# Optimization experiments

Measured on AMD Instinct MI355X. Metric: run time of the kernel, lower is better.

## Reference

```python
import jax, jax.numpy as jnp
import numpy as np

N_AGENTS, OBS_DIM, HID, ACT_DIM = 8192, 64, 128, 16


def setup_inputs() -> dict:
    key = jax.random.key(0)
    k = jax.random.split(key, 8)
    obs_agents = jax.random.normal(k[0], (N_AGENTS, OBS_DIM), dtype=jnp.float32)
    # binary adjacency, {0,1}, int32 (index/mask semantics, non-differentiable)
    adj = jax.random.randint(k[1], (N_AGENTS, N_AGENTS), 0, 2, dtype=jnp.int32)
    def lin(kk, fan_in, fan_out):
        lim = 1.0 / np.sqrt(fan_in)
        kw, kb = jax.random.split(kk)
        W = jax.random.uniform(kw, (fan_in, fan_out), jnp.float32, -lim, lim)
        b = jax.random.uniform(kb, (fan_out,), jnp.float32, -lim, lim)
        return W, b
    W1, b1 = lin(k[2], OBS_DIM, HID)          # encoder
    W2, b2 = lin(k[3], 2 * HID, HID)          # actor layer 1
    W3, b3 = lin(k[4], HID, ACT_DIM)          # actor layer 2
    return {"obs_agents": obs_agents, "adj": adj,
            "W1": W1, "b1": b1, "W2": W2, "b2": b2, "W3": W3, "b3": b3}


def reference(obs_agents, adj, W1, b1, W2, b2, W3, b3):
    # per-agent encode: h = tanh(obs @ W1 + b1)  -> [N, HID]
    h = jnp.tanh(obs_agents @ W1 + b1)
    # neighbor mean message: mean of h[j] over j with adj[i,j]!=0, zeros if no neighbors
    a = adj.astype(h.dtype)                      # [N, N] binary
    deg = jnp.sum(a, axis=1, keepdims=True)      # [N, 1]
    msg = (a @ h) / jnp.maximum(deg, 1.0)        # zero rows stay zero
    # actor MLP on concat([h, msg])
    combined = jnp.concatenate([h, msg], axis=-1)            # [N, 2*HID]
    hid = jnp.tanh(combined @ W2 + b2)                        # [N, HID]
    logits = hid @ W3 + b3                                    # [N, ACT_DIM]
    return logits
```

## Files before the change

kernel.cpp:

```cpp
#include <hip/hip_runtime.h>
#include <stdint.h>
#include <math.h>

#define NAG 8192
#define NC  128
#define NSPLIT 8
#define LDB2 136

typedef __attribute__((ext_vector_type(8))) short short8;
typedef __attribute__((ext_vector_type(4))) float floatx4;

__device__ __forceinline__ float bf2f(unsigned short u) {
    union { uint32_t i; float f; } v; v.i = ((uint32_t)u) << 16; return v.f;
}
__device__ __forceinline__ unsigned short f2bf(float f) {
    union { float f; uint32_t i; } v; v.f = f;
    uint32_t x = v.i;
    return (unsigned short)((x + 0x7FFFu + ((x >> 16) & 1u)) >> 16);
}
__device__ __forceinline__ unsigned short f2h(float f) {
    union { _Float16 h; unsigned short u; } v; v.h = (_Float16)f; return v.u;
}
__device__ __forceinline__ float h2f(unsigned short u) {
    union { _Float16 h; unsigned short u; } v; v.u = u; return (float)v.h;
}
__device__ __forceinline__ bool detect_f32(const void* W1, int t) {
    const unsigned short* w = (const unsigned short*)W1;
    int l = t & 63, big = 0;
    #pragma unroll
    for (int j = 0; j < 8; ++j) {
        float v = bf2f(w[l * 8 + j]);
        if (!(fabsf(v) <= 1e6f)) big = 1;
    }
    return __ballot(big) != 0ull;
}

__global__ __launch_bounds__(256) void kE_encode(
    const void* __restrict__ obs,
    const void* __restrict__ W1,
    const void* __restrict__ b1,
    float* __restrict__ h_f32,
    unsigned short* __restrict__ hT)
{
    __shared__ float obs_lds[32][68];
    __shared__ unsigned short ht_lds[128][33];
    const int t = threadIdx.x;
    const int abase = blockIdx.x * 32;
    const bool isf = detect_f32(W1, t);

    {
        int a = t >> 3, c0 = (t & 7) * 8;
        if (isf) {
            const float* p = (const float*)obs;
            #pragma unroll
            for (int j = 0; j < 8; ++j)
                obs_lds[a][c0 + j] = p[(size_t)(abase + a) * 64 + c0 + j];
        } else {
            const unsigned short* p = (const unsigned short*)obs;
            #pragma unroll
            for (int j = 0; j < 8; ++j)
                obs_lds[a][c0 + j] = bf2f(p[(size_t)(abase + a) * 64 + c0 + j]);
        }
    }
    __syncthreads();

    const int o = t & 127;
    const int half = t >> 7;
    float acc[16];
    if (isf) {
        const float* Wp = (const float*)W1;
        float bias = ((const float*)b1)[o];
        #pragma unroll
        for (int i = 0; i < 16; ++i) acc[i] = bias;
        for (int k0 = 0; k0 < 64; k0 += 8) {
            float w[8];
            #pragma unroll
            for (int j = 0; j < 8; ++j) w[j] = Wp[(k0 + j) * 128 + o];
            #pragma unroll
            for (int j = 0; j < 8; ++j)
                #pragma unroll
                for (int i = 0; i < 16; ++i)
                    acc[i] = fmaf(obs_lds[half * 16 + i][k0 + j], w[j], acc[i]);
        }
    } else {
        const unsigned short* Wp = (const unsigned short*)W1;
        float bias = bf2f(((const unsigned short*)b1)[o]);
        #pragma unroll
        for (int i = 0; i < 16; ++i) acc[i] = bias;
        for (int k0 = 0; k0 < 64; k0 += 8) {
            float w[8];
            #pragma unroll
            for (int j = 0; j < 8; ++j) w[j] = bf2f(Wp[(k0 + j) * 128 + o]);
            #pragma unroll
            for (int j = 0; j < 8; ++j)
                #pragma unroll
                for (int i = 0; i < 16; ++i)
                    acc[i] = fmaf(obs_lds[half * 16 + i][k0 + j], w[j], acc[i]);
        }
    }
    #pragma unroll
    for (int i = 0; i < 16; ++i) {
        float th = tanhf(acc[i]);
        int a = half * 16 + i;
        h_f32[(size_t)(abase + a) * 128 + o] = th;
        ht_lds[o][a] = f2bf(th);
    }
    __syncthreads();

    for (int p = 0; p < 16; ++p) {
        int n = p * 8 + (t >> 5);
        int a = t & 31;
        hT[(size_t)n * NAG + abase + a] = ht_lds[n][a];
    }
}

__global__ __launch_bounds__(256, 4) void kG_msggemm(
    const int* __restrict__ adj,
    const unsigned short* __restrict__ hT,
    unsigned short* __restrict__ Cp16,
    int* __restrict__ degP)
{
    __shared__ __align__(16) unsigned short Blds[128 * LDB2];
    __shared__ __align__(16) unsigned long long bitsLds[4][16][2];
    const int t = threadIdx.x;
    const int mtile = blockIdx.x & 127;
    const int ks = blockIdx.x >> 7;
    const int row0 = mtile * 64;
    const int kbeg = ks * 1024;

    const int wave = t >> 6, lane = t & 63;
    const int fm = lane & 15, quad = lane >> 4;

    floatx4 acc[8];
    #pragma unroll
    for (int i = 0; i < 8; ++i) acc[i] = (floatx4)0.f;

    const int arow = row0 + wave * 16 + fm;
    const int* wrows = adj + (size_t)(row0 + wave * 16) * NAG + kbeg;
    int dsum = 0;

    for (int ss = 0; ss < 8; ++ss) {
        int va[32];
        #pragma unroll
        for (int i = 0; i < 32; ++i) {
            int r = i >> 1, hh = i & 1;
            va[i] = wrows[(size_t)r * NAG + ss * 128 + hh * 64 + lane];
        }
        if (ss) __syncthreads();
        #pragma unroll
        for (int i = 0; i < 8; ++i) {
            int idx = i * 256 + t;
            int row = idx >> 4, ch = idx & 15;
            uint4 v = *reinterpret_cast<const uint4*>(hT + (size_t)row * NAG + kbeg + ss * 128 + ch * 8);
            *reinterpret_cast<uint4*>(&Blds[row * LDB2 + ch * 8]) = v;
        }
        #pragma unroll
        for (int i = 0; i < 32; ++i) {
            unsigned long long m = __ballot(va[i] != 0);
            if (lane == 0) bitsLds[wave][i >> 1][i & 1] = m;
        }
        __syncthreads();
        int4 a0 = *reinterpret_cast<const int4*>(&bitsLds[wave][fm][0]);
        uint32_t aw[4] = {(uint32_t)a0.x, (uint32_t)a0.y, (uint32_t)a0.z, (uint32_t)a0.w};
        dsum += __popc(aw[0]) + __popc(aw[1]) + __popc(aw[2]) + __popc(aw[3]);
        #pragma unroll
        for (int kw = 0; kw < 4; ++kw) {
            uint32_t b = (aw[kw] >> (quad * 8)) & 0xFFu;
            union { uint32_t u[4]; short8 s; } af;
            #pragma unroll
            for (int p = 0; p < 4; ++p) {
                uint32_t bb = b >> (2 * p);
                af.u[p] = ((bb & 1u) | ((bb & 2u) << 15)) * 0x3F80u;
            }
            #pragma unroll
            for (int j = 0; j < 8; ++j) {
                short8 bf = *reinterpret_cast<const short8*>(&Blds[(j * 16 + fm) * LDB2 + kw * 32 + quad * 8]);
                acc[j] = __builtin_amdgcn_mfma_f32_16x16x32_bf16(af.s, bf, acc[j], 0, 0, 0);
            }
        }
    }

    if (quad == 0) degP[ks * NAG + arow] = dsum;

    unsigned short* out = Cp16 + (size_t)ks * (NAG * NC);
    #pragma unroll
    for (int j = 0; j < 8; ++j) {
        int col = j * 16 + fm;
        #pragma unroll
        for (int r = 0; r < 4; ++r) {
            int row = row0 + wave * 16 + quad * 4 + r;
            out[(size_t)row * NC + col] = f2h(acc[j][r]);
        }
    }
}

__global__ __launch_bounds__(256) void k3_actor(
    const float* __restrict__ h_f32,
    const unsigned short* __restrict__ Cp16,
    const int* __restrict__ degP,
    const void* __restrict__ W1,
    const void* __restrict__ W2,
    const void* __restrict__ b2,
    const void* __restrict__ W3,
    const void* __restrict__ b3,
    void* __restrict__ out)
{
    __shared__ float4 comb4[8][66];
    __shared__ float hid[8][132];
    __shared__ int degs[8][9];
    __shared__ float inv_lds[8];
    const int t = threadIdx.x;
    const int abase = blockIdx.x * 8;
    const bool isf = detect_f32(W1, t);
    const size_t PS = (size_t)NAG * NC;

    if (t < 64) {
        int a = t >> 3, s = t & 7;
        degs[a][s] = degP[s * NAG + abase + a];
    }
    __syncthreads();
    if (t < 8) {
        int d = 0;
        #pragma unroll
        for (int s = 0; s < 8; ++s) d += degs[t][s];
        inv_lds[t] = 1.0f / fmaxf((float)d, 1.0f);
    }
    __syncthreads();

    #pragma unroll
    for (int jj = 0; jj < 2; ++jj) {
        int idx = jj * 256 + t;
        int a = idx >> 6, q = idx & 63;
        float4 v;
        if (q < 32) {
            v = *reinterpret_cast<const float4*>(h_f32 + (size_t)(abase + a) * 128 + q * 4);
        } else {
            int f = (q - 32) * 4;
            float s0 = 0.f, s1 = 0.f, s2 = 0.f, s3 = 0.f;
            #pragma unroll
            for (int s = 0; s < NSPLIT; ++s) {
                ushort4 p = *reinterpret_cast<const ushort4*>(Cp16 + s * PS + (size_t)(abase + a) * NC + f);
                s0 += h2f(p.x); s1 += h2f(p.y); s2 += h2f(p.z); s3 += h2f(p.w);
            }
            float sc = inv_lds[a];
            v = make_float4(s0 * sc, s1 * sc, s2 * sc, s3 * sc);
        }
        comb4[a][q] = v;
    }
    __syncthreads();

    const int o = t & 127, half = t >> 7;
    float acc[4];
    if (isf) {
        const float* Wp = (const float*)W2;
        float bias = ((const float*)b2)[o];
        #pragma unroll
        for (int i = 0; i < 4; ++i) acc[i] = bias;
        for (int cq = 0; cq < 64; ++cq) {
            float w0 = Wp[(cq * 4 + 0) * 128 + o];
            float w1 = Wp[(cq * 4 + 1) * 128 + o];
            float w2 = Wp[(cq * 4 + 2) * 128 + o];
            float w3 = Wp[(cq * 4 + 3) * 128 + o];
            #pragma unroll
            for (int i = 0; i < 4; ++i) {
                float4 v = comb4[half * 4 + i][cq];
                acc[i] = fmaf(v.x, w0, acc[i]);
                acc[i] = fmaf(v.y, w1, acc[i]);
                acc[i] = fmaf(v.z, w2, acc[i]);
                acc[i] = fmaf(v.w, w3, acc[i]);
            }
        }
    } else {
        const unsigned short* Wp = (const unsigned short*)W2;
        float bias = bf2f(((const unsigned short*)b2)[o]);
        #pragma unroll
        for (int i = 0; i < 4; ++i) acc[i] = bias;
        for (int cq = 0; cq < 64; ++cq) {
            float w0 = bf2f(Wp[(cq * 4 + 0) * 128 + o]);
            float w1 = bf2f(Wp[(cq * 4 + 1) * 128 + o]);
            float w2 = bf2f(Wp[(cq * 4 + 2) * 128 + o]);
            float w3 = bf2f(Wp[(cq * 4 + 3) * 128 + o]);
            #pragma unroll
            for (int i = 0; i < 4; ++i) {
                float4 v = comb4[half * 4 + i][cq];
                acc[i] = fmaf(v.x, w0, acc[i]);
                acc[i] = fmaf(v.y, w1, acc[i]);
                acc[i] = fmaf(v.z, w2, acc[i]);
                acc[i] = fmaf(v.w, w3, acc[i]);
            }
        }
    }
    #pragma unroll
    for (int i = 0; i < 4; ++i)
        hid[half * 4 + i][o] = tanhf(acc[i]);
    __syncthreads();

    if (t < 128) {
        const int q = t & 15, ar = t >> 4;
        float l;
        if (isf) {
            const float* Wp = (const float*)W3;
            l = ((const float*)b3)[q];
            #pragma unroll 4
            for (int oo = 0; oo < 128; ++oo)
                l = fmaf(hid[ar][oo], Wp[oo * 16 + q], l);
        } else {
            const unsigned short* Wp = (const unsigned short*)W3;
            l = bf2f(((const unsigned short*)b3)[q]);
            #pragma unroll 4
            for (int oo = 0; oo < 128; ++oo)
                l = fmaf(hid[ar][oo], bf2f(Wp[oo * 16 + q]), l);
        }
        size_t i0 = (size_t)(abase + ar) * 16 + q;
        if (isf) ((float*)out)[i0] = l;
        else     ((unsigned short*)out)[i0] = f2bf(l);
    }
}

extern "C" void kernel_launch(void* const* d_in, const int* in_sizes, int n_in,
                              void* d_out, int out_size, void* d_ws, size_t ws_size,
                              hipStream_t stream) {
    const void* obs = d_in[0];
    const int*  adj = (const int*)d_in[1];
    const void* W1  = d_in[2];
    const void* b1  = d_in[3];
    const void* W2  = d_in[4];
    const void* b2  = d_in[5];
    const void* W3  = d_in[6];
    const void* b3  = d_in[7];

    char* ws = (char*)d_ws;
    unsigned short* hT   = (unsigned short*)(ws);
    float*          h_f32= (float*)(ws + 2097152);
    unsigned short* Cp16 = (unsigned short*)(ws + 6291456);
    int*            degP = (int*)(ws + 23068672);

    hipLaunchKernelGGL(kE_encode, dim3(256), dim3(256), 0, stream,
                       obs, W1, b1, h_f32, hT);
    hipLaunchKernelGGL(kG_msggemm, dim3(1024), dim3(256), 0, stream,
                       adj, hT, Cp16, degP);
    hipLaunchKernelGGL(k3_actor, dim3(1024), dim3(256), 0, stream,
                       h_f32, Cp16, degP, W1, W2, b2, W3, b3, d_out);
}
```

Baseline: 467.3 us.

## Restructure adjacency GEMM with register double-buffering and direct global B loads

Rewrites the message GEMM so each wave handles 32 rows instead of 16, halving the grid. Adjacency values are software-pipelined through two register buffers, so the next 64-column chunk is prefetched while the current one is processed. The B operand (hT) is read straight from global memory into registers rather than staged in LDS, which removes the block-wide __syncthreads. This should cut barrier stalls and reuse each B fragment across two MFMA row tiles, at the cost of more register pressure (launch bounds drop to 2 blocks/SM) and redundant global reads of hT.

```diff
diff --git a/kernel.cpp b/kernel.cpp
--- a/kernel.cpp
+++ b/kernel.cpp
@@ -5,7 +5,6 @@
 #define NAG 8192
 #define NC  128
 #define NSPLIT 8
-#define LDB2 136
 
 typedef __attribute__((ext_vector_type(8))) short short8;
 typedef __attribute__((ext_vector_type(4))) float floatx4;
@@ -23,6 +22,15 @@
 }
 __device__ __forceinline__ float h2f(unsigned short u) {
     union { _Float16 h; unsigned short u; } v; v.u = u; return (float)v.h;
+}
+__device__ __forceinline__ short8 mkaf(uint32_t b) {
+    union { uint32_t u[4]; short8 s; } af;
+    #pragma unroll
+    for (int p = 0; p < 4; ++p) {
+        uint32_t bb = b >> (2 * p);
+        af.u[p] = ((bb & 1u) | ((bb & 2u) << 15)) * 0x3F80u;
+    }
+    return af.s;
 }
 __device__ __forceinline__ bool detect_f32(const void* W1, int t) {
     const unsigned short* w = (const unsigned short*)W1;
@@ -114,73 +122,85 @@
     }
 }
 
-__global__ __launch_bounds__(256, 4) void kG_msggemm(
+__global__ __launch_bounds__(256, 2) void kG_msggemm(
     const int* __restrict__ adj,
     const unsigned short* __restrict__ hT,
     unsigned short* __restrict__ Cp16,
     int* __restrict__ degP)
 {
-    __shared__ __align__(16) unsigned short Blds[128 * LDB2];
-    __shared__ __align__(16) unsigned long long bitsLds[4][16][2];
+    __shared__ unsigned long long bitsLds[4][32];
     const int t = threadIdx.x;
-    const int mtile = blockIdx.x & 127;
-    const int ks = blockIdx.x >> 7;
-    const int row0 = mtile * 64;
+    const int mtile = blockIdx.x & 63;
+    const int ks = blockIdx.x >> 6;
     const int kbeg = ks * 1024;
-
     const int wave = t >> 6, lane = t & 63;
     const int fm = lane & 15, quad = lane >> 4;
-
-    floatx4 acc[8];
-    #pragma unroll
-    for (int i = 0; i < 8; ++i) acc[i] = (floatx4)0.f;
-
-    const int arow = row0 + wave * 16 + fm;
-    const int* wrows = adj + (size_t)(row0 + wave * 16) * NAG + kbeg;
-    int dsum = 0;
-
-    for (int ss = 0; ss < 8; ++ss) {
-        int va[32];
-        #pragma unroll
-        for (int i = 0; i < 32; ++i) {
-            int r = i >> 1, hh = i & 1;
-            va[i] = wrows[(size_t)r * NAG + ss * 128 + hh * 64 + lane];
-        }
-        if (ss) __syncthreads();
-        #pragma unroll
-        for (int i = 0; i < 8; ++i) {
-            int idx = i * 256 + t;
-            int row = idx >> 4, ch = idx & 15;
-            uint4 v = *reinterpret_cast<const uint4*>(hT + (size_t)row * NAG + kbeg + ss * 128 + ch * 8);
-            *reinterpret_cast<uint4*>(&Blds[row * LDB2 + ch * 8]) = v;
-        }
-        #pragma unroll
-        for (int i = 0; i < 32; ++i) {
-            unsigned long long m = __ballot(va[i] != 0);
-            if (lane == 0) bitsLds[wave][i >> 1][i & 1] = m;
-        }
-        __syncthreads();
-        int4 a0 = *reinterpret_cast<const int4*>(&bitsLds[wave][fm][0]);
-        uint32_t aw[4] = {(uint32_t)a0.x, (uint32_t)a0.y, (uint32_t)a0.z, (uint32_t)a0.w};
-        dsum += __popc(aw[0]) + __popc(aw[1]) + __popc(aw[2]) + __popc(aw[3]);
-        #pragma unroll
-        for (int kw = 0; kw < 4; ++kw) {
-            uint32_t b = (aw[kw] >> (quad * 8)) & 0xFFu;
-            union { uint32_t u[4]; short8 s; } af;
-            #pragma unroll
-            for (int p = 0; p < 4; ++p) {
-                uint32_t bb = b >> (2 * p);
-                af.u[p] = ((bb & 1u) | ((bb & 2u) << 15)) * 0x3F80u;
-            }
+    const int row0w = mtile * 128 + wave * 32;
+
+    floatx4 acc0[8], acc1[8];
+    #pragma unroll
+    for (int i = 0; i < 8; ++i) { acc0[i] = (floatx4)0.f; acc1[i] = (floatx4)0.f; }
+
+    const int* ap = adj + (size_t)row0w * NAG + kbeg + lane;
+    const unsigned short* hp = hT + (size_t)fm * NAG + kbeg + quad * 8;
+    int d0 = 0, d1 = 0;
+
+    int vaA[32], vaB[32];
+    #pragma unroll
+    for (int r = 0; r < 32; ++r) vaA[r] = ap[(size_t)r * NAG];
+
+    auto STEP = [&](int (&vc)[32], int (&vn)[32], int hs) {
+        const int cofs = hs * 64;
+        short8 b0[8];
+        #pragma unroll
+        for (int j = 0; j < 8; ++j)
+            b0[j] = *reinterpret_cast<const short8*>(hp + (size_t)(j * 16) * NAG + cofs);
+        if (hs < 15) {
+            #pragma unroll
+            for (int r = 0; r < 32; ++r)
+                vn[r] = ap[(size_t)r * NAG + cofs + 64];
+        }
+        #pragma unroll
+        for (int r = 0; r < 32; ++r) {
+            unsigned long long m = __ballot(vc[r] != 0);
+            if (lane == 0) bitsLds[wave][r] = m;
+        }
+        unsigned long long m0 = bitsLds[wave][fm];
+        unsigned long long m1 = bitsLds[wave][16 + fm];
+        d0 += __popcll(m0);
+        d1 += __popcll(m1);
+        {
+            short8 a00 = mkaf(((uint32_t)m0) >> (quad * 8));
+            short8 a01 = mkaf(((uint32_t)m1) >> (quad * 8));
             #pragma unroll
             for (int j = 0; j < 8; ++j) {
-                short8 bf = *reinterpret_cast<const short8*>(&Blds[(j * 16 + fm) * LDB2 + kw * 32 + quad * 8]);
-                acc[j] = __builtin_amdgcn_mfma_f32_16x16x32_bf16(af.s, bf, acc[j], 0, 0, 0);
-            }
-        }
-    }
-
-    if (quad == 0) degP[ks * NAG + arow] = dsum;
+                acc0[j] = __builtin_amdgcn_mfma_f32_16x16x32_bf16(a00, b0[j], acc0[j], 0, 0, 0);
+                acc1[j] = __builtin_amdgcn_mfma_f32_16x16x32_bf16(a01, b0[j], acc1[j], 0, 0, 0);
+            }
+        }
+        {
+            short8 b1v[8];
+            #pragma unroll
+            for (int j = 0; j < 8; ++j)
+                b1v[j] = *reinterpret_cast<const short8*>(hp + (size_t)(j * 16) * NAG + cofs + 32);
+            short8 a10 = mkaf(((uint32_t)(m0 >> 32)) >> (quad * 8));
+            short8 a11 = mkaf(((uint32_t)(m1 >> 32)) >> (quad * 8));
+            #pragma unroll
+            for (int j = 0; j < 8; ++j) {
+                acc0[j] = __builtin_amdgcn_mfma_f32_16x16x32_bf16(a10, b1v[j], acc0[j], 0, 0, 0);
+                acc1[j] = __builtin_amdgcn_mfma_f32_16x16x32_bf16(a11, b1v[j], acc1[j], 0, 0, 0);
+            }
+        }
+    };
+
+    #pragma unroll 1
+    for (int h2 = 0; h2 < 8; ++h2) {
+        STEP(vaA, vaB, 2 * h2);
+        STEP(vaB, vaA, 2 * h2 + 1);
+    }
+
+    if (quad == 0)      degP[ks * NAG + row0w + fm]      = d0;
+    else if (quad == 1) degP[ks * NAG + row0w + 16 + fm] = d1;
 
     unsigned short* out = Cp16 + (size_t)ks * (NAG * NC);
     #pragma unroll
@@ -188,8 +208,9 @@
         int col = j * 16 + fm;
         #pragma unroll
         for (int r = 0; r < 4; ++r) {
-            int row = row0 + wave * 16 + quad * 4 + r;
-            out[(size_t)row * NC + col] = f2h(acc[j][r]);
+            int row0r = row0w + quad * 4 + r;
+            out[(size_t)row0r * NC + col]        = f2h(acc0[j][r]);
+            out[(size_t)(row0r + 16) * NC + col] = f2h(acc1[j][r]);
         }
     }
 }
@@ -337,7 +358,7 @@
 
     hipLaunchKernelGGL(kE_encode, dim3(256), dim3(256), 0, stream,
                        obs, W1, b1, h_f32, hT);
-    hipLaunchKernelGGL(kG_msggemm, dim3(1024), dim3(256), 0, stream,
+    hipLaunchKernelGGL(kG_msggemm, dim3(512), dim3(256), 0, stream,
                        adj, hT, Cp16, degP);
     hipLaunchKernelGGL(k3_actor, dim3(1024), dim3(256), 0, stream,
                        h_f32, Cp16, degP, W1, W2, b2, W3, b3, d_out);
```

Result: no change. 469.8 us (+0.5%).
